# Optimization experiments

Hardware: AMD Instinct MI355X
Metric: run time of the kernel (lower is better)

Reference implementation:

```python
import jax, jax.numpy as jnp
import numpy as np
from jax import lax

L, E, H, V, T = 4096, 512, 512, 50000, 32
START, END = 0, 1
NEG = -10000.0


def setup_inputs() -> dict:
    key = jax.random.key(0)
    ks = jax.random.split(key, 16)
    s = 0.1  # keep activations in a sane range
    inp = {
        'sentence': jax.random.randint(ks[0], (L,), 0, V, dtype=jnp.int32),
        'embed':  jax.random.normal(ks[1], (V, E)) * s,
        'w_ih_f': jax.random.normal(ks[2], (4 * H, E)) * s,
        'w_hh_f': jax.random.normal(ks[3], (4 * H, H)) * s,
        'b_ih_f': jax.random.normal(ks[4], (4 * H,)) * s,
        'b_hh_f': jax.random.normal(ks[5], (4 * H,)) * s,
        'w_ih_b': jax.random.normal(ks[6], (4 * H, E)) * s,
        'w_hh_b': jax.random.normal(ks[7], (4 * H, H)) * s,
        'b_ih_b': jax.random.normal(ks[8], (4 * H,)) * s,
        'b_hh_b': jax.random.normal(ks[9], (4 * H,)) * s,
        'w_out':  jax.random.normal(ks[10], (T, 2 * H)) * s,
        'b_out':  jax.random.normal(ks[11], (T,)) * s,
        'h0':     jax.random.normal(ks[13], (2, H)),
        'c0':     jax.random.normal(ks[14], (2, H)),
    }
    trans = jax.random.normal(ks[12], (T, T))
    # CRF constraints: never transition into START, never leave from END
    trans = trans.at[START, :].set(NEG).at[:, END].set(NEG)
    inp['trans'] = trans
    return inp


def _lstm_dir(xs, w_ih, w_hh, b_ih, b_hh, h0, c0, reverse):
    # xs: (L, E). PyTorch gate order: i, f, g, o. Precompute input projection.
    x_proj = xs @ w_ih.T + (b_ih + b_hh)  # (L, 4H)

    def step(carry, xp):
        h, c = carry
        gates = xp + h @ w_hh.T
        i, f, g, o = jnp.split(gates, 4)
        i, f, o = jax.nn.sigmoid(i), jax.nn.sigmoid(f), jax.nn.sigmoid(o)
        g = jnp.tanh(g)
        c = f * c + i * g
        h = o * jnp.tanh(c)
        return (h, c), h

    _, hs = lax.scan(step, (h0, c0), x_proj, reverse=reverse)
    return hs  # (L, H)


def reference(sentence, embed, w_ih_f, w_hh_f, b_ih_f, b_hh_f,
              w_ih_b, w_hh_b, b_ih_b, b_hh_b, w_out, b_out, trans, h0, c0):
    xs = embed[sentence]  # (L, E)
    hs_f = _lstm_dir(xs, w_ih_f, w_hh_f, b_ih_f, b_hh_f, h0[0], c0[0], False)
    hs_b = _lstm_dir(xs, w_ih_b, w_hh_b, b_ih_b, b_hh_b, h0[1], c0[1], True)
    feats = jnp.concatenate([hs_f, hs_b], axis=1) @ w_out.T + b_out  # (L, T)

    # Viterbi forward: trans[next, prev]
    init_v = jnp.full((T,), NEG).at[START].set(0.0)

    def vstep(fv, feat):
        scores = trans + fv[None, :]          # (T_next, T_prev)
        bptr = jnp.argmax(scores, axis=1)     # (T,)
        fv_new = jnp.max(scores, axis=1) + feat
        return fv_new, bptr

    fv, bptrs = lax.scan(vstep, init_v, feats)  # bptrs: (L, T)
    terminal = fv + trans[END]
    score = jnp.max(terminal)
    last_tag = jnp.argmax(terminal)

    # Backtrace (reverse scan): path[L-1]=last_tag, path[i]=bptrs[i+1][path[i+1]]
    def back(tag, bp):
        return bp[tag], tag

    _, path = lax.scan(back, last_tag, bptrs, reverse=True)  # (L,)
    return score, path
```

## Files before the change

### kernel.cpp

```cpp
#include <hip/hip_runtime.h>
#include <stdint.h>

#define L_SEQ 4096
#define E_DIM 512
#define H_DIM 512
#define G_DIM 2048
#define NTAG  32

typedef unsigned long long u64;
typedef unsigned short     u16;
typedef unsigned char      u8;

__device__ __forceinline__ float bf2f(u16 u) {
    union { unsigned int i; float f; } v; v.i = ((unsigned int)u) << 16; return v.f;
}
__device__ __forceinline__ bool sniff_f32(const void* trans_raw) {
    const u16* p = (const u16*)trans_raw;
    return p[0] != p[1];
}
__device__ __forceinline__ float ldf(const void* base, long idx, bool isf32) {
    if (isf32) return ((const float*)base)[idx];
    return bf2f(((const u16*)base)[idx]);
}
__device__ __forceinline__ void unpack8_bf16(const u16* src, float* dst) {
    uint4 p = *(const uint4*)src;
    dst[0] = __uint_as_float(p.x << 16); dst[1] = __uint_as_float(p.x & 0xffff0000u);
    dst[2] = __uint_as_float(p.y << 16); dst[3] = __uint_as_float(p.y & 0xffff0000u);
    dst[4] = __uint_as_float(p.z << 16); dst[5] = __uint_as_float(p.z & 0xffff0000u);
    dst[6] = __uint_as_float(p.w << 16); dst[7] = __uint_as_float(p.w & 0xffff0000u);
}

__global__ __launch_bounds__(256) void k_xproj(
    const int* __restrict__ sent, const void* __restrict__ embed,
    const void* __restrict__ w_ih_f, const void* __restrict__ b_ih_f, const void* __restrict__ b_hh_f,
    const void* __restrict__ w_ih_b, const void* __restrict__ b_ih_b, const void* __restrict__ b_hh_b,
    const void* __restrict__ trans_raw,
    float* __restrict__ xp_f, float* __restrict__ xp_b)
{
    const bool isf32 = sniff_f32(trans_raw);
    const int dir = (int)blockIdx.y;
    const void* W  = dir ? w_ih_b : w_ih_f;
    const void* bi = dir ? b_ih_b : b_ih_f;
    const void* bh = dir ? b_hh_b : b_hh_f;
    float* xp = dir ? xp_b : xp_f;
    const int m0 = (int)blockIdx.x * 16;
    const int tid = (int)threadIdx.x;

    __shared__ float xs[16][520];
    __shared__ float wl[16][520];

    {
        const int r = tid >> 4, c0 = (tid & 15) * 32;
        const long row = sent[m0 + r];
        if (isf32) {
            const float* src = (const float*)embed + row * E_DIM + c0;
            #pragma unroll
            for (int i = 0; i < 32; i += 4) *(float4*)&xs[r][c0 + i] = *(const float4*)(src + i);
        } else {
            const u16* src = (const u16*)embed + row * E_DIM + c0;
            #pragma unroll
            for (int i = 0; i < 32; i += 8) unpack8_bf16(src + i, &xs[r][c0 + i]);
        }
    }
    __syncthreads();

    const int mi = tid >> 4, gi = tid & 15;
    for (int gb = 0; gb < 128; ++gb) {
        const int g0 = gb * 16;
        {
            const int r = tid >> 4, c0 = (tid & 15) * 32;
            if (isf32) {
                const float* src = (const float*)W + (long)(g0 + r) * E_DIM + c0;
                #pragma unroll
                for (int i = 0; i < 32; i += 4) *(float4*)&wl[r][c0 + i] = *(const float4*)(src + i);
            } else {
                const u16* src = (const u16*)W + (long)(g0 + r) * E_DIM + c0;
                #pragma unroll
                for (int i = 0; i < 32; i += 8) unpack8_bf16(src + i, &wl[r][c0 + i]);
            }
        }
        __syncthreads();

        float acc = 0.f;
        #pragma unroll 4
        for (int k = 0; k < E_DIM; k += 4) {
            const float4 xv = *(const float4*)&xs[mi][k];
            const float4 wv = *(const float4*)&wl[gi][k];
            acc = fmaf(xv.x, wv.x, acc); acc = fmaf(xv.y, wv.y, acc);
            acc = fmaf(xv.z, wv.z, acc); acc = fmaf(xv.w, wv.w, acc);
        }
        const int g = g0 + gi;
        const float bias = ldf(bi, g, isf32) + ldf(bh, g, isf32);
        xp[(long)(m0 + mi) * G_DIM + g] = acc + bias;
        __syncthreads();
    }
}

__global__ __launch_bounds__(256, 1) void k_lstm(
    const void* __restrict__ w_hh_f, const void* __restrict__ w_hh_b,
    const void* __restrict__ h0, const void* __restrict__ c0,
    const void* __restrict__ trans_raw,
    const float* __restrict__ xp_f, const float* __restrict__ xp_b,
    u64* __restrict__ hsT_f, u64* __restrict__ hsT_b)
{
    const bool isf32 = sniff_f32(trans_raw);
    const int dir = (int)(blockIdx.x >> 4);
    const int wg  = (int)(blockIdx.x & 15);
    const int j0  = wg * 32;
    const void* Whh = dir ? w_hh_b : w_hh_f;
    const float* xp = dir ? xp_b : xp_f;
    u64* hsT        = dir ? hsT_b : hsT_f;

    const int tid  = (int)threadIdx.x;
    const int wv   = tid >> 6;
    const int lane = tid & 63;
    const int rs   = lane >> 3;
    const int ks   = lane & 7;

    __shared__ float h_lds[8 * 68];
    __shared__ float gates_lds[4 * 32];

    float wreg[4][64];
    #pragma unroll
    for (int rl = 0; rl < 4; ++rl) {
        const long roff = (long)(wv * H_DIM + j0 + rs * 4 + rl) * H_DIM + ks * 64;
        if (isf32) {
            const float* wrow = (const float*)Whh + roff;
            #pragma unroll
            for (int b = 0; b < 16; ++b) *(float4*)&wreg[rl][b * 4] = *(const float4*)(wrow + b * 4);
        } else {
            const u16* wrow = (const u16*)Whh + roff;
            #pragma unroll
            for (int b = 0; b < 8; ++b) unpack8_bf16(wrow + b * 8, &wreg[rl][b * 8]);
        }
    }

    {
        const int w0 = tid * 2;
        h_lds[w0 + ((w0 >> 6) << 2)]     = ldf(h0, dir * H_DIM + w0, isf32);
        h_lds[w0 + 1 + ((w0 >> 6) << 2)] = ldf(h0, dir * H_DIM + w0 + 1, isf32);
    }
    float cst = 0.f;
    if (wv == 0 && lane < 32) cst = ldf(c0, dir * H_DIM + j0 + lane, isf32);

    int t = dir ? (L_SEQ - 1) : 0;
    float xpn0 = 0, xpn1 = 0, xpn2 = 0, xpn3 = 0;
    if (wv == 0 && lane < 32) {
        const float* xr = xp + (long)t * G_DIM + j0 + lane;
        xpn0 = xr[0]; xpn1 = xr[H_DIM]; xpn2 = xr[2 * H_DIM]; xpn3 = xr[3 * H_DIM];
    }
    __syncthreads();

    #pragma unroll 1
    for (int k = 0; k < L_SEQ; ++k) {
        t = dir ? (L_SEQ - 1 - k) : k;
        const float xc0 = xpn0, xc1 = xpn1, xc2 = xpn2, xc3 = xpn3;
        if (wv == 0 && lane < 32 && k + 1 < L_SEQ) {
            const int nt = dir ? (t - 1) : (t + 1);
            const float* xr = xp + (long)nt * G_DIM + j0 + lane;
            xpn0 = xr[0]; xpn1 = xr[H_DIM]; xpn2 = xr[2 * H_DIM]; xpn3 = xr[3 * H_DIM];
        }

        float a0 = 0, a1 = 0, a2 = 0, a3 = 0;
        const float4* hb = (const float4*)(h_lds + ks * 68);
        #pragma unroll
        for (int q = 0; q < 16; ++q) {
            const float4 hv = hb[q];
            a0 = fmaf(wreg[0][4*q+0], hv.x, a0); a0 = fmaf(wreg[0][4*q+1], hv.y, a0);
            a0 = fmaf(wreg[0][4*q+2], hv.z, a0); a0 = fmaf(wreg[0][4*q+3], hv.w, a0);
            a1 = fmaf(wreg[1][4*q+0], hv.x, a1); a1 = fmaf(wreg[1][4*q+1], hv.y, a1);
            a1 = fmaf(wreg[1][4*q+2], hv.z, a1); a1 = fmaf(wreg[1][4*q+3], hv.w, a1);
            a2 = fmaf(wreg[2][4*q+0], hv.x, a2); a2 = fmaf(wreg[2][4*q+1], hv.y, a2);
            a2 = fmaf(wreg[2][4*q+2], hv.z, a2); a2 = fmaf(wreg[2][4*q+3], hv.w, a2);
            a3 = fmaf(wreg[3][4*q+0], hv.x, a3); a3 = fmaf(wreg[3][4*q+1], hv.y, a3);
            a3 = fmaf(wreg[3][4*q+2], hv.z, a3); a3 = fmaf(wreg[3][4*q+3], hv.w, a3);
        }
        #pragma unroll
        for (int m = 1; m < 8; m <<= 1) {
            a0 += __shfl_xor(a0, m); a1 += __shfl_xor(a1, m);
            a2 += __shfl_xor(a2, m); a3 += __shfl_xor(a3, m);
        }
        if (ks == 0) {
            float4 g4; g4.x = a0; g4.y = a1; g4.z = a2; g4.w = a3;
            *(float4*)&gates_lds[wv * 32 + rs * 4] = g4;
        }
        __syncthreads();

        if (wv == 0 && lane < 32) {
            const int jl = lane;
            const float gi = gates_lds[jl]      + xc0;
            const float gf = gates_lds[32 + jl] + xc1;
            const float gg = gates_lds[64 + jl] + xc2;
            const float go = gates_lds[96 + jl] + xc3;
            const float iv = 1.f / (1.f + expf(-gi));
            const float fo = 1.f / (1.f + expf(-gf));
            const float gv = tanhf(gg);
            const float ov = 1.f / (1.f + expf(-go));
            cst = fo * cst + iv * gv;
            const float hv = ov * tanhf(cst);
            const int j = j0 + jl;
            h_lds[j + ((j >> 6) << 2)] = hv;
            const u64 pk = (((u64)(unsigned)(k + 1)) << 32) | (u64)__float_as_uint(hv);
            __hip_atomic_store(&hsT[(long)t * H_DIM + j], pk,
                               __ATOMIC_RELAXED, __HIP_MEMORY_SCOPE_AGENT);
        }

        if (k + 1 < L_SEQ && tid < 240) {
            int w0 = tid * 2; if (w0 >= j0) w0 += 32;
            const unsigned tagv = (unsigned)(k + 1);
            u64* p0 = &hsT[(long)t * H_DIM + w0];
            u64 v0, v1;
            do { v0 = __hip_atomic_load(p0,     __ATOMIC_RELAXED, __HIP_MEMORY_SCOPE_AGENT); }
            while ((unsigned)(v0 >> 32) != tagv);
            do { v1 = __hip_atomic_load(p0 + 1, __ATOMIC_RELAXED, __HIP_MEMORY_SCOPE_AGENT); }
            while ((unsigned)(v1 >> 32) != tagv);
            const int d0 = w0 + ((w0 >> 6) << 2);
            h_lds[d0]     = __uint_as_float((unsigned)v0);
            h_lds[d0 + 1] = __uint_as_float((unsigned)v1);
        }
        __syncthreads();
    }
}

__global__ __launch_bounds__(256) void k_feats(
    const u64* __restrict__ hsT_f, const u64* __restrict__ hsT_b,
    const void* __restrict__ w_out, const void* __restrict__ b_out,
    const void* __restrict__ trans_raw, float* __restrict__ feats)
{
    const bool isf32 = sniff_f32(trans_raw);
    const int n  = (int)threadIdx.x & 31;
    const int tl = (int)threadIdx.x >> 5;
    const int t  = (int)blockIdx.x * 8 + tl;
    const float* hf  = (const float*)(hsT_f + (long)t * H_DIM);
    const float* hbp = (const float*)(hsT_b + (long)t * H_DIM);
    float acc = ldf(b_out, n, isf32);
    if (isf32) {
        const float* wf = (const float*)w_out + (long)n * 1024;
        const float* wb = wf + 512;
        #pragma unroll 4
        for (int j2 = 0; j2 < 256; ++j2) {
            acc = fmaf(hf [4 * j2],     wf[2 * j2],     acc);
            acc = fmaf(hf [4 * j2 + 2], wf[2 * j2 + 1], acc);
            acc = fmaf(hbp[4 * j2],     wb[2 * j2],     acc);
            acc = fmaf(hbp[4 * j2 + 2], wb[2 * j2 + 1], acc);
        }
    } else {
        const unsigned int* wf = (const unsigned int*)((const u16*)w_out + (long)n * 1024);
        const unsigned int* wb = (const unsigned int*)((const u16*)w_out + (long)n * 1024 + 512);
        #pragma unroll 4
        for (int j2 = 0; j2 < 256; ++j2) {
            const unsigned int wp = wf[j2];
            const unsigned int wq = wb[j2];
            acc = fmaf(hf [4 * j2],     __uint_as_float(wp << 16),         acc);
            acc = fmaf(hf [4 * j2 + 2], __uint_as_float(wp & 0xffff0000u), acc);
            acc = fmaf(hbp[4 * j2],     __uint_as_float(wq << 16),         acc);
            acc = fmaf(hbp[4 * j2 + 2], __uint_as_float(wq & 0xffff0000u), acc);
        }
    }
    feats[(long)t * 32 + n] = acc;
}

__global__ __launch_bounds__(64) void k_viterbi(
    const float* __restrict__ feats, const void* __restrict__ trans_raw,
    u8* __restrict__ bptr, float* __restrict__ out)
{
    const bool isf32 = sniff_f32(trans_raw);
    const int lane = (int)threadIdx.x;
    const int n = lane & 31, half = lane >> 5;
    __shared__ float fv[32];
    __shared__ u8 mlds[64 * 32];
    __shared__ u8 entry[64];

    float tr[16];
    #pragma unroll
    for (int i = 0; i < 16; ++i) tr[i] = ldf(trans_raw, n * 32 + half * 16 + i, isf32);
    const float tr_end = ldf(trans_raw, 32 + n, isf32);

    if (half == 0) fv[n] = (n == 0) ? 0.f : -10000.f;
    __syncthreads();

    float fnext = feats[n];
    #pragma unroll 1
    for (int tt = 0; tt < L_SEQ; ++tt) {
        const float fcur = fnext;
        const int nt = (tt + 1 < L_SEQ) ? tt + 1 : tt;
        fnext = feats[(long)nt * 32 + n];

        float best = -3.4e38f; int bp = 0;
        #pragma unroll
        for (int i = 0; i < 16; ++i) {
            const float cand = tr[i] + fv[half * 16 + i];
            if (cand > best) { best = cand; bp = half * 16 + i; }
        }
        const float ob = __shfl_xor(best, 32);
        const int  obp = __shfl_xor(bp, 32);
        if (ob > best || (ob == best && obp < bp)) { best = ob; bp = obp; }

        if (half == 0) {
            fv[n] = best + fcur;
            bptr[(long)tt * 32 + n] = (u8)bp;
        }
        __syncthreads();
    }

    float term = (half == 0) ? (fv[n] + tr_end) : -3.4e38f;
    int   ti   = (half == 0) ? n : 1000;
    #pragma unroll
    for (int m = 1; m < 64; m <<= 1) {
        const float ov = __shfl_xor(term, m);
        const int   oi = __shfl_xor(ti, m);
        if (ov > term || (ov == term && oi < ti)) { term = ov; ti = oi; }
    }
    if (lane == 0) out[0] = term;
    __syncthreads();

    unsigned cur[32];
    #pragma unroll
    for (int ch = 0; ch < 32; ++ch) cur[ch] = (unsigned)ch;
    const int cbase = lane * 64;
    for (int s = 63; s >= 0; --s) {
        const u8* row = bptr + (long)(cbase + s) * 32;
        #pragma unroll
        for (int ch = 0; ch < 32; ++ch) cur[ch] = row[cur[ch]];
    }
    #pragma unroll
    for (int ch = 0; ch < 32; ++ch) mlds[lane * 32 + ch] = (u8)cur[ch];
    __syncthreads();

    if (lane == 0) {
        int tag = ti;
        for (int c = 63; c >= 0; --c) { entry[c] = (u8)tag; tag = mlds[c * 32 + tag]; }
    }
    __syncthreads();

    {
        int tag = entry[lane];
        for (int s = 63; s >= 0; --s) {
            const int gidx = cbase + s;
            out[1 + gidx] = (float)tag;
            tag = bptr[(long)gidx * 32 + tag];
        }
    }
}

extern "C" void kernel_launch(void* const* d_in, const int* in_sizes, int n_in,
                              void* d_out, int out_size, void* d_ws, size_t ws_size,
                              hipStream_t stream)
{
    (void)in_sizes; (void)n_in; (void)out_size; (void)ws_size;
    const int* sent  = (const int*)d_in[0];
    const void* embed  = d_in[1];
    const void* w_ih_f = d_in[2];
    const void* w_hh_f = d_in[3];
    const void* b_ih_f = d_in[4];
    const void* b_hh_f = d_in[5];
    const void* w_ih_b = d_in[6];
    const void* w_hh_b = d_in[7];
    const void* b_ih_b = d_in[8];
    const void* b_hh_b = d_in[9];
    const void* w_out  = d_in[10];
    const void* b_out  = d_in[11];
    const void* h0     = d_in[12];
    const void* c0     = d_in[13];
    const void* trans  = d_in[14];

    char* ws = (char*)d_ws;
    float* xp_f  = (float*)(ws);
    float* xp_b  = (float*)(ws + (32ull << 20));
    u64*   hsT_f = (u64*)(ws + (64ull << 20));
    u64*   hsT_b = (u64*)(ws + (80ull << 20));
    float* feats = (float*)(ws);
    u8*    bptr  = (u8*)(ws + (1ull << 20));

    k_xproj<<<dim3(256, 2), 256, 0, stream>>>(sent, embed,
        w_ih_f, b_ih_f, b_hh_f, w_ih_b, b_ih_b, b_hh_b, trans, xp_f, xp_b);
    k_lstm<<<32, 256, 0, stream>>>(w_hh_f, w_hh_b, h0, c0, trans, xp_f, xp_b, hsT_f, hsT_b);
    k_feats<<<512, 256, 0, stream>>>(hsT_f, hsT_b, w_out, b_out, trans, feats);
    k_viterbi<<<1, 64, 0, stream>>>(feats, trans, bptr, (float*)d_out);
}
```

Before: 13.07 ms.

## Spread LSTM recurrence over 64 blocks, fast activations, register-based Viterbi

The recurrent LSTM kernel now splits each direction over 32 workgroups of 16 hidden units instead of 16 of 32. Each thread holds 2 weight rows instead of 4, gates are combined with shuffles rather than through LDS and a barrier, and one lane per unit applies the activations. Sigmoid and tanh use hardware exp2/rcp approximations, and cross-block polling now waits on three values at once. The Viterbi loop keeps forward scores in registers and broadcasts them with shuffles, which removes shared memory and per-step barriers. In exchange there are more blocks taking part in the per-step global handshake, and the approximate activations may lose some precision.

```diff
diff --git a/kernel.cpp b/kernel.cpp
--- a/kernel.cpp
+++ b/kernel.cpp
@@ -28,6 +28,14 @@
     dst[2] = __uint_as_float(p.y << 16); dst[3] = __uint_as_float(p.y & 0xffff0000u);
     dst[4] = __uint_as_float(p.z << 16); dst[5] = __uint_as_float(p.z & 0xffff0000u);
     dst[6] = __uint_as_float(p.w << 16); dst[7] = __uint_as_float(p.w & 0xffff0000u);
+}
+
+#define LOG2E 1.44269504088896340736f
+__device__ __forceinline__ float fsig(float x) {
+    return __builtin_amdgcn_rcpf(1.f + __builtin_amdgcn_exp2f(-x * LOG2E));
+}
+__device__ __forceinline__ float ftanh(float x) {
+    return 1.f - 2.f * __builtin_amdgcn_rcpf(1.f + __builtin_amdgcn_exp2f(x * (2.f * LOG2E)));
 }
 
 __global__ __launch_bounds__(256) void k_xproj(
@@ -104,26 +112,26 @@
     u64* __restrict__ hsT_f, u64* __restrict__ hsT_b)
 {
     const bool isf32 = sniff_f32(trans_raw);
-    const int dir = (int)(blockIdx.x >> 4);
-    const int wg  = (int)(blockIdx.x & 15);
-    const int j0  = wg * 32;
+    const int dir = (int)(blockIdx.x >> 5);
+    const int wg  = (int)(blockIdx.x & 31);
+    const int j0  = wg * 16;
     const void* Whh = dir ? w_hh_b : w_hh_f;
     const float* xp = dir ? xp_b : xp_f;
     u64* hsT        = dir ? hsT_b : hsT_f;
 
-    const int tid  = (int)threadIdx.x;
-    const int wv   = tid >> 6;
-    const int lane = tid & 63;
-    const int rs   = lane >> 3;
-    const int ks   = lane & 7;
-
-    __shared__ float h_lds[8 * 68];
-    __shared__ float gates_lds[4 * 32];
-
-    float wreg[4][64];
-    #pragma unroll
-    for (int rl = 0; rl < 4; ++rl) {
-        const long roff = (long)(wv * H_DIM + j0 + rs * 4 + rl) * H_DIM + ks * 64;
+    const int tid = (int)threadIdx.x;
+    const int rp  = tid >> 3;
+    const int ks  = tid & 7;
+    const int d   = rp >> 1;
+    const int gp  = rp & 1;
+    const int g0r = gp * 2;
+
+    __shared__ float h_lds[512 + 32];
+
+    float wreg[2][64];
+    #pragma unroll
+    for (int rl = 0; rl < 2; ++rl) {
+        const long roff = (long)((g0r + rl) * H_DIM + j0 + d) * H_DIM + ks * 64;
         if (isf32) {
             const float* wrow = (const float*)Whh + roff;
             #pragma unroll
@@ -140,28 +148,43 @@
         h_lds[w0 + ((w0 >> 6) << 2)]     = ldf(h0, dir * H_DIM + w0, isf32);
         h_lds[w0 + 1 + ((w0 >> 6) << 2)] = ldf(h0, dir * H_DIM + w0 + 1, isf32);
     }
+
+    const bool is_act = ((tid & 15) == 0);
+    const int  jown   = j0 + d;
     float cst = 0.f;
-    if (wv == 0 && lane < 32) cst = ldf(c0, dir * H_DIM + j0 + lane, isf32);
+    if (is_act) cst = ldf(c0, dir * H_DIM + jown, isf32);
+
+    const int b16 = tid >> 4, off = tid & 15;
+    const int pidx = is_act ? -1 : (b16 * 15 + off - 1);
+    int jw0 = 0, jw1 = 0, jw2 = -1;
+    if (pidx >= 0) {
+        const int w0 = 2 * pidx, w1 = 2 * pidx + 1;
+        jw0 = w0 + (w0 >= j0 ? 16 : 0);
+        jw1 = w1 + (w1 >= j0 ? 16 : 0);
+        if (pidx < 16) { const int w2 = 480 + pidx; jw2 = w2 + (w2 >= j0 ? 16 : 0); }
+    }
 
     int t = dir ? (L_SEQ - 1) : 0;
-    float xpn0 = 0, xpn1 = 0, xpn2 = 0, xpn3 = 0;
-    if (wv == 0 && lane < 32) {
-        const float* xr = xp + (long)t * G_DIM + j0 + lane;
-        xpn0 = xr[0]; xpn1 = xr[H_DIM]; xpn2 = xr[2 * H_DIM]; xpn3 = xr[3 * H_DIM];
+    float xc0 = 0, xc1 = 0, xc2 = 0, xc3 = 0, xn0 = 0, xn1 = 0, xn2 = 0, xn3 = 0;
+    if (is_act) {
+        const float* xr = xp + (long)t * G_DIM + jown;
+        xn0 = xr[0]; xn1 = xr[H_DIM]; xn2 = xr[2 * H_DIM]; xn3 = xr[3 * H_DIM];
     }
     __syncthreads();
 
     #pragma unroll 1
     for (int k = 0; k < L_SEQ; ++k) {
         t = dir ? (L_SEQ - 1 - k) : k;
-        const float xc0 = xpn0, xc1 = xpn1, xc2 = xpn2, xc3 = xpn3;
-        if (wv == 0 && lane < 32 && k + 1 < L_SEQ) {
-            const int nt = dir ? (t - 1) : (t + 1);
-            const float* xr = xp + (long)nt * G_DIM + j0 + lane;
-            xpn0 = xr[0]; xpn1 = xr[H_DIM]; xpn2 = xr[2 * H_DIM]; xpn3 = xr[3 * H_DIM];
-        }
-
-        float a0 = 0, a1 = 0, a2 = 0, a3 = 0;
+        if (is_act) {
+            xc0 = xn0; xc1 = xn1; xc2 = xn2; xc3 = xn3;
+            if (k + 1 < L_SEQ) {
+                const int nt = dir ? (t - 1) : (t + 1);
+                const float* xr = xp + (long)nt * G_DIM + jown;
+                xn0 = xr[0]; xn1 = xr[H_DIM]; xn2 = xr[2 * H_DIM]; xn3 = xr[3 * H_DIM];
+            }
+        }
+
+        float a0 = 0, a1 = 0;
         const float4* hb = (const float4*)(h_lds + ks * 68);
         #pragma unroll
         for (int q = 0; q < 16; ++q) {
@@ -170,53 +193,43 @@
             a0 = fmaf(wreg[0][4*q+2], hv.z, a0); a0 = fmaf(wreg[0][4*q+3], hv.w, a0);
             a1 = fmaf(wreg[1][4*q+0], hv.x, a1); a1 = fmaf(wreg[1][4*q+1], hv.y, a1);
             a1 = fmaf(wreg[1][4*q+2], hv.z, a1); a1 = fmaf(wreg[1][4*q+3], hv.w, a1);
-            a2 = fmaf(wreg[2][4*q+0], hv.x, a2); a2 = fmaf(wreg[2][4*q+1], hv.y, a2);
-            a2 = fmaf(wreg[2][4*q+2], hv.z, a2); a2 = fmaf(wreg[2][4*q+3], hv.w, a2);
-            a3 = fmaf(wreg[3][4*q+0], hv.x, a3); a3 = fmaf(wreg[3][4*q+1], hv.y, a3);
-            a3 = fmaf(wreg[3][4*q+2], hv.z, a3); a3 = fmaf(wreg[3][4*q+3], hv.w, a3);
         }
         #pragma unroll
-        for (int m = 1; m < 8; m <<= 1) {
-            a0 += __shfl_xor(a0, m); a1 += __shfl_xor(a1, m);
-            a2 += __shfl_xor(a2, m); a3 += __shfl_xor(a3, m);
-        }
-        if (ks == 0) {
-            float4 g4; g4.x = a0; g4.y = a1; g4.z = a2; g4.w = a3;
-            *(float4*)&gates_lds[wv * 32 + rs * 4] = g4;
-        }
-        __syncthreads();
-
-        if (wv == 0 && lane < 32) {
-            const int jl = lane;
-            const float gi = gates_lds[jl]      + xc0;
-            const float gf = gates_lds[32 + jl] + xc1;
-            const float gg = gates_lds[64 + jl] + xc2;
-            const float go = gates_lds[96 + jl] + xc3;
-            const float iv = 1.f / (1.f + expf(-gi));
-            const float fo = 1.f / (1.f + expf(-gf));
-            const float gv = tanhf(gg);
-            const float ov = 1.f / (1.f + expf(-go));
+        for (int m = 1; m < 8; m <<= 1) { a0 += __shfl_xor(a0, m); a1 += __shfl_xor(a1, m); }
+        const float b0 = __shfl_xor(a0, 8);
+        const float b1 = __shfl_xor(a1, 8);
+
+        if (is_act) {
+            const float iv = fsig(a0 + xc0);
+            const float fo = fsig(a1 + xc1);
+            const float gv = ftanh(b0 + xc2);
+            const float ov = fsig(b1 + xc3);
             cst = fo * cst + iv * gv;
-            const float hv = ov * tanhf(cst);
-            const int j = j0 + jl;
-            h_lds[j + ((j >> 6) << 2)] = hv;
-            const u64 pk = (((u64)(unsigned)(k + 1)) << 32) | (u64)__float_as_uint(hv);
-            __hip_atomic_store(&hsT[(long)t * H_DIM + j], pk,
+            const float hv2 = ov * ftanh(cst);
+            h_lds[jown + ((jown >> 6) << 2)] = hv2;
+            const u64 pk = (((u64)(unsigned)(k + 1)) << 32) | (u64)__float_as_uint(hv2);
+            __hip_atomic_store(&hsT[(long)t * H_DIM + jown], pk,
                                __ATOMIC_RELAXED, __HIP_MEMORY_SCOPE_AGENT);
         }
 
-        if (k + 1 < L_SEQ && tid < 240) {
-            int w0 = tid * 2; if (w0 >= j0) w0 += 32;
+        if (k + 1 < L_SEQ && pidx >= 0) {
             const unsigned tagv = (unsigned)(k + 1);
-            u64* p0 = &hsT[(long)t * H_DIM + w0];
-            u64 v0, v1;
-            do { v0 = __hip_atomic_load(p0,     __ATOMIC_RELAXED, __HIP_MEMORY_SCOPE_AGENT); }
-            while ((unsigned)(v0 >> 32) != tagv);
-            do { v1 = __hip_atomic_load(p0 + 1, __ATOMIC_RELAXED, __HIP_MEMORY_SCOPE_AGENT); }
-            while ((unsigned)(v1 >> 32) != tagv);
-            const int d0 = w0 + ((w0 >> 6) << 2);
-            h_lds[d0]     = __uint_as_float((unsigned)v0);
-            h_lds[d0 + 1] = __uint_as_float((unsigned)v1);
+            u64* pa0 = &hsT[(long)t * H_DIM + jw0];
+            u64* pa1 = &hsT[(long)t * H_DIM + jw1];
+            u64* pa2 = (jw2 >= 0) ? &hsT[(long)t * H_DIM + jw2] : pa0;
+            u64 v0 = 0, v1 = 0, v2 = 0;
+            bool q0 = false, q1 = false, q2 = (jw2 < 0);
+            do {
+                if (!q0) { v0 = __hip_atomic_load(pa0, __ATOMIC_RELAXED, __HIP_MEMORY_SCOPE_AGENT); }
+                if (!q1) { v1 = __hip_atomic_load(pa1, __ATOMIC_RELAXED, __HIP_MEMORY_SCOPE_AGENT); }
+                if (!q2) { v2 = __hip_atomic_load(pa2, __ATOMIC_RELAXED, __HIP_MEMORY_SCOPE_AGENT); }
+                q0 = q0 || ((unsigned)(v0 >> 32) == tagv);
+                q1 = q1 || ((unsigned)(v1 >> 32) == tagv);
+                q2 = q2 || ((unsigned)(v2 >> 32) == tagv);
+            } while (!(q0 && q1 && q2));
+            h_lds[jw0 + ((jw0 >> 6) << 2)] = __uint_as_float((unsigned)v0);
+            h_lds[jw1 + ((jw1 >> 6) << 2)] = __uint_as_float((unsigned)v1);
+            if (jw2 >= 0) h_lds[jw2 + ((jw2 >> 6) << 2)] = __uint_as_float((unsigned)v2);
         }
         __syncthreads();
     }
@@ -267,7 +280,6 @@
     const bool isf32 = sniff_f32(trans_raw);
     const int lane = (int)threadIdx.x;
     const int n = lane & 31, half = lane >> 5;
-    __shared__ float fv[32];
     __shared__ u8 mlds[64 * 32];
     __shared__ u8 entry[64];
 
@@ -276,9 +288,7 @@
     for (int i = 0; i < 16; ++i) tr[i] = ldf(trans_raw, n * 32 + half * 16 + i, isf32);
     const float tr_end = ldf(trans_raw, 32 + n, isf32);
 
-    if (half == 0) fv[n] = (n == 0) ? 0.f : -10000.f;
-    __syncthreads();
-
+    float fvreg = (n == 0) ? 0.f : -10000.f;
     float fnext = feats[n];
     #pragma unroll 1
     for (int tt = 0; tt < L_SEQ; ++tt) {
@@ -289,21 +299,18 @@
         float best = -3.4e38f; int bp = 0;
         #pragma unroll
         for (int i = 0; i < 16; ++i) {
-            const float cand = tr[i] + fv[half * 16 + i];
-            if (cand > best) { best = cand; bp = half * 16 + i; }
+            const float c = tr[i] + __shfl(fvreg, half * 16 + i);
+            if (c > best) { best = c; bp = half * 16 + i; }
         }
         const float ob = __shfl_xor(best, 32);
         const int  obp = __shfl_xor(bp, 32);
         if (ob > best || (ob == best && obp < bp)) { best = ob; bp = obp; }
 
-        if (half == 0) {
-            fv[n] = best + fcur;
-            bptr[(long)tt * 32 + n] = (u8)bp;
-        }
-        __syncthreads();
-    }
-
-    float term = (half == 0) ? (fv[n] + tr_end) : -3.4e38f;
+        fvreg = best + fcur;
+        if (half == 0) bptr[(long)tt * 32 + n] = (u8)bp;
+    }
+
+    float term = (half == 0) ? (fvreg + tr_end) : -3.4e38f;
     int   ti   = (half == 0) ? n : 1000;
     #pragma unroll
     for (int m = 1; m < 64; m <<= 1) {
@@ -374,7 +381,7 @@
 
     k_xproj<<<dim3(256, 2), 256, 0, stream>>>(sent, embed,
         w_ih_f, b_ih_f, b_hh_f, w_ih_b, b_ih_b, b_hh_b, trans, xp_f, xp_b);
-    k_lstm<<<32, 256, 0, stream>>>(w_hh_f, w_hh_b, h0, c0, trans, xp_f, xp_b, hsT_f, hsT_b);
+    k_lstm<<<64, 256, 0, stream>>>(w_hh_f, w_hh_b, h0, c0, trans, xp_f, xp_b, hsT_f, hsT_b);
     k_feats<<<512, 256, 0, stream>>>(hsT_f, hsT_b, w_out, b_out, trans, feats);
     k_viterbi<<<1, 64, 0, stream>>>(feats, trans, bptr, (float*)d_out);
 }
```

Result: faster. 12.58 ms (-3.8%).
